# Performance work log

Hardware: AMD Instinct MI355X
Metric: run time of the kernel (lower is better)

## Reference

```python
import jax, jax.numpy as jnp
import numpy as np

BN_EPS = 1e-5


def setup_inputs() -> dict:
    key = jax.random.key(0)
    ks = jax.random.split(key, 16)
    N, E, D, H = 100000, 1200000, 64, 128
    return {
        "x": jax.random.normal(ks[0], (N, D), dtype=jnp.float32),
        "edge_index": jax.random.randint(ks[1], (2, E), 0, N, dtype=jnp.int64),
        "edge_weight": jax.random.uniform(ks[2], (E,), dtype=jnp.float32),
        "edge_features": jax.random.normal(ks[3], (E, 16), dtype=jnp.float32),
        "adj": jnp.zeros((1,), dtype=jnp.float32),
        "T": 1,
        "bn_gamma": jax.random.uniform(ks[4], (D,), dtype=jnp.float32) + 0.5,
        "bn_beta": jax.random.normal(ks[5], (D,), dtype=jnp.float32) * 0.1,
        "W_l": jax.random.normal(ks[6], (D, H), dtype=jnp.float32) / np.sqrt(D),
        "b_l": jax.random.normal(ks[7], (H,), dtype=jnp.float32) * 0.01,
        "W_r": jax.random.normal(ks[8], (D, H), dtype=jnp.float32) / np.sqrt(D),
        "W1": jax.random.normal(ks[9], (H, 16), dtype=jnp.float32) / np.sqrt(H),
        "b1": jax.random.normal(ks[10], (16,), dtype=jnp.float32) * 0.01,
        "W2": jax.random.normal(ks[11], (16, 2), dtype=jnp.float32) / 4.0,
        "b2": jax.random.normal(ks[12], (2,), dtype=jnp.float32) * 0.01,
    }


def reference(x, edge_index, edge_weight, edge_features, adj, T,
              bn_gamma, bn_beta, W_l, b_l, W_r, W1, b1, W2, b2):
    # edge_weight, edge_features, adj, T are accepted but unused, matching the
    # original module's forward.
    N = x.shape[0]
    # BatchNorm1d (training mode: batch statistics, biased variance)
    mean = jnp.mean(x, axis=0)
    var = jnp.var(x, axis=0)
    xn = (x - mean) * jax.lax.rsqrt(var + BN_EPS) * bn_gamma + bn_beta

    # SAGEConv with mean aggregation: out = lin_l(mean_{j->i} x_j) + lin_r(x_i)
    src, dst = edge_index[0], edge_index[1]
    agg = jax.ops.segment_sum(xn[src], dst, num_segments=N)  # [N, D]
    deg = jax.ops.segment_sum(jnp.ones_like(dst, dtype=xn.dtype), dst,
                              num_segments=N)
    agg = agg / jnp.maximum(deg, 1.0)[:, None]
    h = agg @ W_l + b_l + xn @ W_r  # [N, H]
    h = jax.nn.relu(h)

    # classifier head: Linear(H,16) -> ReLU -> Linear(16,2)
    out = jax.nn.relu(h @ W1 + b1) @ W2 + b2  # [N, 2]
    return out
```

## Files before the change

kernel.cpp:

```cpp
#include <hip/hip_runtime.h>

#define FEAT 64
#define HDIM 128
#define BN_EPS 1e-5f

#define BSH 7
#define NB_MAX 1024
#define SCHUNK 4096
#define SEG 4096
#define CAP 2048

#define PSOFF 1280
#define PQOFF (PSOFF + 65536)
#define WCOFF (PQOFF + 65536)
#define XNOFF (WCOFF + 8192)

typedef __attribute__((ext_vector_type(8))) short bf16x8;
typedef __attribute__((ext_vector_type(4))) float f32x4;

#define GL16(gp, lp)                                                        \
    __builtin_amdgcn_global_load_lds(                                       \
        (const __attribute__((address_space(1))) unsigned int*)(gp),        \
        (__attribute__((address_space(3))) unsigned int*)(lp), 16, 0, 0)

__device__ inline unsigned short f2bf(float f) {
    union { float f; unsigned int u; } v;
    v.f = f;
    unsigned int r = (v.u + 0x7FFFu + ((v.u >> 16) & 1u)) >> 16;
    return (unsigned short)r;
}
__device__ inline float bf2f(unsigned short b) {
    union { unsigned int u; float f; } v;
    v.u = ((unsigned int)b) << 16;
    return v.f;
}

__global__ __launch_bounds__(256) void kA(const float* __restrict__ x,
                                          float* __restrict__ ws,
                                          const float* __restrict__ Wl,
                                          const float* __restrict__ Wr,
                                          unsigned short* __restrict__ Wc,
                                          const int* __restrict__ ei,
                                          int* __restrict__ bktCnt,
                                          int* __restrict__ pairs,
                                          int N, int E, int nb) {
    __shared__ float sd[256], sd2[256];
    __shared__ int hist[NB_MAX];
    __shared__ int base[NB_MAX];
    int blk = blockIdx.x, t = threadIdx.x;
    if (blk < 1024) {
        int col = t & 63, rib = t >> 6;
        float s = 0.f, sq = 0.f;
        for (int r = blk * 4 + rib; r < N; r += 4096) {
            float v = x[(size_t)r * FEAT + col];
            s += v;
            sq += v * v;
        }
        sd[t] = s;
        sd2[t] = sq;
        __syncthreads();
        if (t < 64) {
            s = sd[col] + sd[col + 64] + sd[col + 128] + sd[col + 192];
            sq = sd2[col] + sd2[col + 64] + sd2[col + 128] + sd2[col + 192];
            ws[PSOFF + col * 1024 + blk] = s;
            ws[PQOFF + col * 1024 + blk] = sq;
        }
    } else if (blk < 1088) {
        int id = (blk - 1024) * 256 + t;
        int n = id >> 7, k = id & 127;
        float w = (k < 64) ? Wl[k * HDIM + n] : Wr[(k - 64) * HDIM + n];
        Wc[((k >> 5) * 128 + n) * 32 + (k & 31)] = f2bf(w);
    } else {
        int chunk = blk - 1088;
        int e0 = chunk * SCHUNK;
        int e1 = min(E, e0 + SCHUNK);
        for (int b = t; b < nb; b += 256) hist[b] = 0;
        __syncthreads();
        for (int e = e0 + t; e < e1; e += 256)
            atomicAdd(&hist[((unsigned)ei[E + e]) >> BSH], 1);
        __syncthreads();
        for (int b = t; b < nb; b += 256) {
            int c = hist[b];
            base[b] = c ? atomicAdd(&bktCnt[b], c) : 0;
            hist[b] = 0;
        }
        __syncthreads();
        for (int e = e0 + t; e < e1; e += 256) {
            int src = ei[e];
            int dst = ei[E + e];
            int b = ((unsigned)dst) >> BSH;
            int off = atomicAdd(&hist[b], 1);
            int pos = base[b] + off;
            if (pos < CAP) pairs[b * CAP + pos] = (src << BSH) | (dst & 127);
        }
    }
}

__global__ __launch_bounds__(256) void kB(float* __restrict__ ws,
                                          const float* __restrict__ gamma,
                                          const float* __restrict__ beta, int N) {
    __shared__ float r1[256], r2[256];
    int blk = blockIdx.x, t = threadIdx.x;
    const float* pS = ws + PSOFF + blk * 1024;
    const float* pQ = ws + PQOFF + blk * 1024;
    float s = 0.f, q = 0.f;
    for (int j = t; j < 1024; j += 256) { s += pS[j]; q += pQ[j]; }
    r1[t] = s;
    r2[t] = q;
    __syncthreads();
    for (int off = 128; off > 0; off >>= 1) {
        if (t < off) { r1[t] += r1[t + off]; r2[t] += r2[t + off]; }
        __syncthreads();
    }
    if (t == 0) {
        float invN = 1.0f / (float)N;
        float mean = r1[0] * invN;
        float var = r2[0] * invN - mean * mean;
        float sc = rsqrtf(var + BN_EPS) * gamma[blk];
        ws[128 + blk] = sc;
        ws[192 + blk] = beta[blk] - mean * sc;
    }
}

__global__ __launch_bounds__(256) void k3_norm(const float* __restrict__ x,
                                               const float* __restrict__ ws,
                                               unsigned short* __restrict__ xn, int N) {
    const float4* x4 = (const float4*)x;
    ushort4* o4 = (ushort4*)xn;
    int n4 = N * (FEAT / 4);
    int stride = gridDim.x * blockDim.x;
    for (int i = blockIdx.x * blockDim.x + threadIdx.x; i < n4; i += stride) {
        int cg = (i & 15) << 2;
        float4 v = x4[i];
        float4 sc = *(const float4*)(ws + 128 + cg);
        float4 sh = *(const float4*)(ws + 192 + cg);
        ushort4 o;
        o.x = f2bf(v.x * sc.x + sh.x);
        o.y = f2bf(v.y * sc.y + sh.y);
        o.z = f2bf(v.z * sc.z + sh.z);
        o.w = f2bf(v.w * sc.w + sh.w);
        o4[i] = o;
    }
}

__global__ __launch_bounds__(512) void kda(const int* __restrict__ pairs,
                                           const int* __restrict__ bktCnt,
                                           const unsigned short* __restrict__ xn,
                                           unsigned short* __restrict__ agg, int N) {
    __shared__ int sidx[SEG];
    __shared__ int cnt[128], nstart[128], ncur[128];
    int b = blockIdx.x;
    int base = b << BSH;
    int total = min(bktCnt[b], CAP);
    int bs = b * CAP, be = bs + total;
    int t = threadIdx.x;
    int lane = t & 63, wv = t >> 6;
    int part = lane & 7, slot = lane >> 3;

    if (total <= SEG) {
        if (t < 128) cnt[t] = 0;
        __syncthreads();
        for (int i = bs + t; i < be; i += 512)
            atomicAdd(&cnt[pairs[i] & 127], 1);
        __syncthreads();
        if (wv == 0) {
            int c0 = cnt[lane], c1 = cnt[64 + lane];
            int a = c0, d = c1;
#pragma unroll
            for (int off = 1; off < 64; off <<= 1) {
                int ta = __shfl_up(a, off);
                int td = __shfl_up(d, off);
                if (lane >= off) { a += ta; d += td; }
            }
            int totA = __shfl(a, 63);
            d += totA;
            nstart[lane] = a - c0;
            ncur[lane] = a - c0;
            nstart[64 + lane] = d - c1;
            ncur[64 + lane] = d - c1;
        }
        __syncthreads();
        for (int i = bs + t; i < be; i += 512) {
            int p = pairs[i];
            int nid = p & 127;
            int pos = atomicAdd(&ncur[nid], 1);
            sidx[pos] = (p >> BSH) << 6;
        }
        __syncthreads();

        int nA = wv * 16 + slot;
        int nB = nA + 8;
        int stA = nstart[nA], dA = cnt[nA];
        int stB = nstart[nB], dB = cnt[nB];
        float accA[8], accB[8];
#pragma unroll
        for (int j = 0; j < 8; j++) { accA[j] = 0.f; accB[j] = 0.f; }
        bf16x8 vA = {}, vB = {};
        for (int e = 0;; e++) {
            bool pA = e < dA, pB = e < dB;
            if (!__any(pA || pB)) break;
            if (pA) vA = *(const bf16x8*)(xn + sidx[stA + e] + part * 8);
            if (pB) vB = *(const bf16x8*)(xn + sidx[stB + e] + part * 8);
#pragma unroll
            for (int j = 0; j < 8; j++) {
                accA[j] += pA ? bf2f((unsigned short)vA[j]) : 0.f;
                accB[j] += pB ? bf2f((unsigned short)vB[j]) : 0.f;
            }
        }
        int nodeA = base + nA;
        int nodeB = base + nB;
        if (nodeA < N) {
            float dinv = (dA > 0) ? (1.0f / (float)dA) : 0.0f;
            union { bf16x8 v; unsigned short u[8]; } o;
#pragma unroll
            for (int j = 0; j < 8; j++) o.u[j] = f2bf(accA[j] * dinv);
            *(bf16x8*)(agg + (size_t)nodeA * FEAT + part * 8) = o.v;
        }
        if (nodeB < N) {
            float dinv = (dB > 0) ? (1.0f / (float)dB) : 0.0f;
            union { bf16x8 v; unsigned short u[8]; } o;
#pragma unroll
            for (int j = 0; j < 8; j++) o.u[j] = f2bf(accB[j] * dinv);
            *(bf16x8*)(agg + (size_t)nodeB * FEAT + part * 8) = o.v;
        }
    } else {
        for (int ni = wv; ni < 128; ni += 8) {
            int node = base + ni;
            if (node >= N) continue;
            float acc = 0.f;
            int deg = 0;
            for (int i = bs; i < be; i++) {
                int p = pairs[i];
                if ((p & 127) == ni) {
                    acc += bf2f(xn[((p >> BSH) << 6) + lane]);
                    deg++;
                }
            }
            float dinv = (deg > 0) ? (1.0f / (float)deg) : 0.0f;
            agg[(size_t)node * FEAT + lane] = f2bf(acc * dinv);
        }
    }
}

__global__ __launch_bounds__(256, 3) void k5_gemm(
    const unsigned short* __restrict__ agg, const unsigned short* __restrict__ xn,
    const unsigned short* __restrict__ Wc, const float* __restrict__ bl,
    const float* __restrict__ W1, const float* __restrict__ b1,
    const float* __restrict__ W2, const float* __restrict__ b2,
    float* __restrict__ out, int N) {
    __shared__ unsigned char tile[16384];
    __shared__ float hq[64][17];
    int t = threadIdx.x;
    int lane = t & 63;
    int wv = t >> 6;
    int rh = wv & 1;
    int ch = wv >> 1;
    int c = lane & 15;
    int q = lane >> 4;
    int row0 = blockIdx.x * 64;

    {
        int rrow = t >> 3;
        int sseg = t & 7;
#pragma unroll
        for (int r = 0; r < 2; r++) {
            int row = r * 32 + rrow;
            int grow = min(row0 + row, N - 1);
            int seg = sseg ^ (row & 7);
            unsigned ldso = (unsigned)(r * 4096 + wv * 1024);
            GL16(agg + (size_t)grow * 64 + seg * 8, &tile[ldso]);
            GL16(xn + (size_t)grow * 64 + seg * 8, &tile[8192 + ldso]);
        }
    }
    __syncthreads();

    f32x4 acc[2][4];
    f32x4 z = {0.f, 0.f, 0.f, 0.f};
#pragma unroll
    for (int rt = 0; rt < 2; rt++)
#pragma unroll
        for (int nt = 0; nt < 4; nt++) acc[rt][nt] = z;

#pragma unroll
    for (int kt = 0; kt < 4; kt++) {
        bf16x8 bfr[4];
#pragma unroll
        for (int nt = 0; nt < 4; nt++) {
            int col = ch * 64 + nt * 16 + c;
            bfr[nt] = *(const bf16x8*)(Wc + ((size_t)kt * 128 + col) * 32 + q * 8);
        }
        const unsigned char* abase = &tile[(kt < 2) ? 0 : 8192];
        int sg = (kt & 1) * 4 + q;
        bf16x8 af[2];
#pragma unroll
        for (int rt = 0; rt < 2; rt++) {
            int rowL = rh * 32 + rt * 16 + c;
            af[rt] = *(const bf16x8*)&abase[rowL * 128 + ((sg ^ (rowL & 7)) << 4)];
        }
#pragma unroll
        for (int rt = 0; rt < 2; rt++)
#pragma unroll
            for (int nt = 0; nt < 4; nt++)
                acc[rt][nt] = __builtin_amdgcn_mfma_f32_16x16x32_bf16(
                    af[rt], bfr[nt], acc[rt][nt], 0, 0, 0);
    }

    float bln[4];
    float4 w1v[4][4];
#pragma unroll
    for (int nt = 0; nt < 4; nt++) {
        int col = ch * 64 + nt * 16 + c;
        bln[nt] = bl[col];
        const float4* wp = (const float4*)(W1 + col * 16);
#pragma unroll
        for (int qq = 0; qq < 4; qq++) w1v[nt][qq] = wp[qq];
    }
    int m = ((c & 1) << 3) | ((c & 2) << 1) | ((c & 4) >> 1) | ((c & 8) >> 3);
    float b1v = b1[m];
    float w2x = W2[2 * m];
    float w2y = W2[2 * m + 1];

    float sv[2][4];
#pragma unroll
    for (int rt = 0; rt < 2; rt++) {
#pragma unroll
        for (int r = 0; r < 4; r++) {
            float tp[16];
#pragma unroll
            for (int j = 0; j < 16; j++) tp[j] = 0.f;
#pragma unroll
            for (int nt = 0; nt < 4; nt++) {
                float hv = fmaxf(acc[rt][nt][r] + bln[nt], 0.f);
#pragma unroll
                for (int qq = 0; qq < 4; qq++) {
                    tp[qq * 4 + 0] += hv * w1v[nt][qq].x;
                    tp[qq * 4 + 1] += hv * w1v[nt][qq].y;
                    tp[qq * 4 + 2] += hv * w1v[nt][qq].z;
                    tp[qq * 4 + 3] += hv * w1v[nt][qq].w;
                }
            }
            float u[8];
#pragma unroll
            for (int k = 0; k < 8; k++) {
                float keep = (c & 1) ? tp[k + 8] : tp[k];
                float send = (c & 1) ? tp[k] : tp[k + 8];
                u[k] = keep + __shfl_xor(send, 1);
            }
            float v4[4];
#pragma unroll
            for (int k = 0; k < 4; k++) {
                float keep = (c & 2) ? u[k + 4] : u[k];
                float send = (c & 2) ? u[k] : u[k + 4];
                v4[k] = keep + __shfl_xor(send, 2);
            }
            float w2v[2];
#pragma unroll
            for (int k = 0; k < 2; k++) {
                float keep = (c & 4) ? v4[k + 2] : v4[k];
                float send = (c & 4) ? v4[k] : v4[k + 2];
                w2v[k] = keep + __shfl_xor(send, 4);
            }
            {
                float keep = (c & 8) ? w2v[1] : w2v[0];
                float send = (c & 8) ? w2v[0] : w2v[1];
                sv[rt][r] = keep + __shfl_xor(send, 8);
            }
        }
    }

    if (ch == 0) {
#pragma unroll
        for (int rt = 0; rt < 2; rt++)
#pragma unroll
            for (int r = 0; r < 4; r++)
                hq[rh * 32 + rt * 16 + q * 4 + r][m] = sv[rt][r];
    }
    __syncthreads();
    if (ch == 1) {
        float b2x = b2[0], b2y = b2[1];
#pragma unroll
        for (int rt = 0; rt < 2; rt++) {
#pragma unroll
            for (int r = 0; r < 4; r++) {
                int row = rh * 32 + rt * 16 + q * 4 + r;
                float tm = sv[rt][r] + hq[row][m] + b1v;
                tm = fmaxf(tm, 0.f);
                float o0 = tm * w2x;
                float o1 = tm * w2y;
#pragma unroll
                for (int mk = 1; mk < 16; mk <<= 1) {
                    o0 += __shfl_xor(o0, mk);
                    o1 += __shfl_xor(o1, mk);
                }
                if (c == 0) {
                    int rowg = row0 + row;
                    if (rowg < N) {
                        out[(size_t)rowg * 2 + 0] = o0 + b2x;
                        out[(size_t)rowg * 2 + 1] = o1 + b2y;
                    }
                }
            }
        }
    }
}

extern "C" void kernel_launch(void* const* d_in, const int* in_sizes, int n_in,
                              void* d_out, int out_size, void* d_ws, size_t ws_size,
                              hipStream_t stream) {
    const float* x = (const float*)d_in[0];
    const int* ei = (const int*)d_in[1];
    const float* gamma = (const float*)d_in[6];
    const float* beta = (const float*)d_in[7];
    const float* Wl = (const float*)d_in[8];
    const float* bl = (const float*)d_in[9];
    const float* Wr = (const float*)d_in[10];
    const float* W1 = (const float*)d_in[11];
    const float* b1 = (const float*)d_in[12];
    const float* W2 = (const float*)d_in[13];
    const float* b2 = (const float*)d_in[14];

    int N = in_sizes[0] / FEAT;
    int E = in_sizes[1] / 2;
    int nb = (N + 127) >> BSH;
    int sbin = (E + SCHUNK - 1) / SCHUNK;

    float* ws = (float*)d_ws;
    int* wsi = (int*)d_ws;
    int bcOff = 256;
    int aggOff = XNOFF + N * 32;
    int pairsOff = aggOff + N * 32;

    unsigned short* xnp = (unsigned short*)(ws + XNOFF);
    unsigned short* aggp = (unsigned short*)(ws + aggOff);
    unsigned short* wcp = (unsigned short*)(ws + WCOFF);
    int* bktCnt = wsi + bcOff;
    int* pairs = wsi + pairsOff;

    float* out = (float*)d_out;

    hipMemsetAsync(bktCnt, 0, NB_MAX * sizeof(int), stream);
    hipLaunchKernelGGL(kA, dim3(1088 + sbin), dim3(256), 0, stream,
                       x, ws, Wl, Wr, wcp, ei, bktCnt, pairs, N, E, nb);
    hipLaunchKernelGGL(kB, dim3(64), dim3(256), 0, stream, ws, gamma, beta, N);
    hipLaunchKernelGGL(k3_norm, dim3(2048), dim3(256), 0, stream, x, ws, xnp, N);
    hipLaunchKernelGGL(kda, dim3(nb), dim3(512), 0, stream,
                       pairs, bktCnt, xnp, aggp, N);
    hipLaunchKernelGGL(k5_gemm, dim3((N + 63) / 64), dim3(256), 0, stream,
                       aggp, xnp, wcp, bl, W1, b1, W2, b2, out, N);
}
```

Measured before the change: 249.5 us.

## Reorder kA blocks to schedule edge bucketing first and vectorize BN stats

Moves the edge-bucketing blocks to the front of the fused kA grid so the longer atomic-heavy scatter work starts before the BN-statistics and weight-conversion blocks. The BN partial-sum branch now reads contiguous row ranges with float4 loads and reduces with wave shuffles. Each chunk also walks its bucket-count atomics from a rotated starting bucket to spread contention on bktCnt. The reordering relies on block dispatch order for overlap, and the new row-range split changes the summation order of the statistics.

```diff
diff --git a/kernel.cpp b/kernel.cpp
--- a/kernel.cpp
+++ b/kernel.cpp
@@ -43,35 +43,14 @@
                                           const int* __restrict__ ei,
                                           int* __restrict__ bktCnt,
                                           int* __restrict__ pairs,
-                                          int N, int E, int nb) {
-    __shared__ float sd[256], sd2[256];
+                                          int N, int E, int nb, int sbin) {
+    __shared__ float4 sS[4][16];
+    __shared__ float4 sQ[4][16];
     __shared__ int hist[NB_MAX];
     __shared__ int base[NB_MAX];
     int blk = blockIdx.x, t = threadIdx.x;
-    if (blk < 1024) {
-        int col = t & 63, rib = t >> 6;
-        float s = 0.f, sq = 0.f;
-        for (int r = blk * 4 + rib; r < N; r += 4096) {
-            float v = x[(size_t)r * FEAT + col];
-            s += v;
-            sq += v * v;
-        }
-        sd[t] = s;
-        sd2[t] = sq;
-        __syncthreads();
-        if (t < 64) {
-            s = sd[col] + sd[col + 64] + sd[col + 128] + sd[col + 192];
-            sq = sd2[col] + sd2[col + 64] + sd2[col + 128] + sd2[col + 192];
-            ws[PSOFF + col * 1024 + blk] = s;
-            ws[PQOFF + col * 1024 + blk] = sq;
-        }
-    } else if (blk < 1088) {
-        int id = (blk - 1024) * 256 + t;
-        int n = id >> 7, k = id & 127;
-        float w = (k < 64) ? Wl[k * HDIM + n] : Wr[(k - 64) * HDIM + n];
-        Wc[((k >> 5) * 128 + n) * 32 + (k & 31)] = f2bf(w);
-    } else {
-        int chunk = blk - 1088;
+    if (blk < sbin) {
+        int chunk = blk;
         int e0 = chunk * SCHUNK;
         int e1 = min(E, e0 + SCHUNK);
         for (int b = t; b < nb; b += 256) hist[b] = 0;
@@ -79,7 +58,10 @@
         for (int e = e0 + t; e < e1; e += 256)
             atomicAdd(&hist[((unsigned)ei[E + e]) >> BSH], 1);
         __syncthreads();
-        for (int b = t; b < nb; b += 256) {
+        int rot = (chunk * 131) % nb;
+        for (int j = t; j < nb; j += 256) {
+            int b = j + rot;
+            if (b >= nb) b -= nb;
             int c = hist[b];
             base[b] = c ? atomicAdd(&bktCnt[b], c) : 0;
             hist[b] = 0;
@@ -93,6 +75,56 @@
             int pos = base[b] + off;
             if (pos < CAP) pairs[b * CAP + pos] = (src << BSH) | (dst & 127);
         }
+    } else if (blk < sbin + 1024) {
+        int sblk = blk - sbin;
+        int rpb = (N + 1023) >> 10;
+        int colg = t & 15, rowi = t >> 4;
+        int lane = t & 63, wv = t >> 6;
+        const float4* x4 = (const float4*)x;
+        float4 s4 = {0.f, 0.f, 0.f, 0.f}, q4 = {0.f, 0.f, 0.f, 0.f};
+        int r0 = sblk * rpb;
+        for (int i = rowi; i < rpb; i += 16) {
+            int r = r0 + i;
+            if (r < N) {
+                float4 v = x4[r * 16 + colg];
+                s4.x += v.x; s4.y += v.y; s4.z += v.z; s4.w += v.w;
+                q4.x += v.x * v.x; q4.y += v.y * v.y;
+                q4.z += v.z * v.z; q4.w += v.w * v.w;
+            }
+        }
+#pragma unroll
+        for (int mk = 16; mk <= 32; mk <<= 1) {
+            s4.x += __shfl_xor(s4.x, mk); s4.y += __shfl_xor(s4.y, mk);
+            s4.z += __shfl_xor(s4.z, mk); s4.w += __shfl_xor(s4.w, mk);
+            q4.x += __shfl_xor(q4.x, mk); q4.y += __shfl_xor(q4.y, mk);
+            q4.z += __shfl_xor(q4.z, mk); q4.w += __shfl_xor(q4.w, mk);
+        }
+        if (lane < 16) { sS[wv][lane] = s4; sQ[wv][lane] = q4; }
+        __syncthreads();
+        if (t < 16) {
+            float4 a = sS[0][t], b4 = sQ[0][t];
+#pragma unroll
+            for (int w = 1; w < 4; w++) {
+                a.x += sS[w][t].x; a.y += sS[w][t].y;
+                a.z += sS[w][t].z; a.w += sS[w][t].w;
+                b4.x += sQ[w][t].x; b4.y += sQ[w][t].y;
+                b4.z += sQ[w][t].z; b4.w += sQ[w][t].w;
+            }
+            int c0 = t * 4;
+            ws[PSOFF + (c0 + 0) * 1024 + sblk] = a.x;
+            ws[PSOFF + (c0 + 1) * 1024 + sblk] = a.y;
+            ws[PSOFF + (c0 + 2) * 1024 + sblk] = a.z;
+            ws[PSOFF + (c0 + 3) * 1024 + sblk] = a.w;
+            ws[PQOFF + (c0 + 0) * 1024 + sblk] = b4.x;
+            ws[PQOFF + (c0 + 1) * 1024 + sblk] = b4.y;
+            ws[PQOFF + (c0 + 2) * 1024 + sblk] = b4.z;
+            ws[PQOFF + (c0 + 3) * 1024 + sblk] = b4.w;
+        }
+    } else {
+        int id = (blk - sbin - 1024) * 256 + t;
+        int n = id >> 7, k = id & 127;
+        float w = (k < 64) ? Wl[k * HDIM + n] : Wr[(k - 64) * HDIM + n];
+        Wc[((k >> 5) * 128 + n) * 32 + (k & 31)] = f2bf(w);
     }
 }
 
@@ -439,8 +471,8 @@
     float* out = (float*)d_out;
 
     hipMemsetAsync(bktCnt, 0, NB_MAX * sizeof(int), stream);
-    hipLaunchKernelGGL(kA, dim3(1088 + sbin), dim3(256), 0, stream,
-                       x, ws, Wl, Wr, wcp, ei, bktCnt, pairs, N, E, nb);
+    hipLaunchKernelGGL(kA, dim3(sbin + 1088), dim3(256), 0, stream,
+                       x, ws, Wl, Wr, wcp, ei, bktCnt, pairs, N, E, nb, sbin);
     hipLaunchKernelGGL(kB, dim3(64), dim3(256), 0, stream, ws, gamma, beta, N);
     hipLaunchKernelGGL(k3_norm, dim3(2048), dim3(256), 0, stream, x, ws, xnp, N);
     hipLaunchKernelGGL(kda, dim3(nb), dim3(512), 0, stream,
```

New measurement: 249.0 us. Within noise of the previous version (-0.2%).
